# Kernel tuning notes

Measured on AMD Instinct MI355X. Metric: run time of the kernel, lower is better.

The kernel has to match this reference:

```python
import jax, jax.numpy as jnp
import numpy as np
import math

D_MODEL = 512
NHEAD = 8
N_LAYERS = 3
D_FF = 2048
INPUT_DIM = 128
NUM_CLASSES = 64
FACTOR = 5


def setup_inputs() -> dict:
    key = jax.random.key(0)
    ks = jax.random.split(key, 24)
    s = 0.02
    d, f, nl = D_MODEL, D_FF, N_LAYERS
    inp = {
        "x": jax.random.normal(ks[0], (4, 1024, INPUT_DIM), dtype=jnp.float32),
        "W_emb": jax.random.normal(ks[1], (INPUT_DIM, d), dtype=jnp.float32) * s,
        "b_emb": jnp.zeros((d,), jnp.float32),
        "Wq": jax.random.normal(ks[2], (nl, d, d), dtype=jnp.float32) * s,
        "bq": jnp.zeros((nl, d), jnp.float32),
        "Wk": jax.random.normal(ks[3], (nl, d, d), dtype=jnp.float32) * s,
        "bk": jnp.zeros((nl, d), jnp.float32),
        "Wv": jax.random.normal(ks[4], (nl, d, d), dtype=jnp.float32) * s,
        "bv": jnp.zeros((nl, d), jnp.float32),
        "Wo": jax.random.normal(ks[5], (nl, d, d), dtype=jnp.float32) * s,
        "bo": jnp.zeros((nl, d), jnp.float32),
        "ln1_g": jnp.ones((nl, d), jnp.float32),
        "ln1_b": jnp.zeros((nl, d), jnp.float32),
        "W1": jax.random.normal(ks[6], (nl, d, f), dtype=jnp.float32) * s,
        "b1": jnp.zeros((nl, f), jnp.float32),
        "W2": jax.random.normal(ks[7], (nl, f, d), dtype=jnp.float32) * s,
        "b2": jnp.zeros((nl, d), jnp.float32),
        "ln2_g": jnp.ones((nl, d), jnp.float32),
        "ln2_b": jnp.zeros((nl, d), jnp.float32),
        "W_dec": jax.random.normal(ks[8], (d, NUM_CLASSES), dtype=jnp.float32) * s,
        "b_dec": jnp.zeros((NUM_CLASSES,), jnp.float32),
    }
    return inp


def _layer_norm(x, g, b, eps=1e-5):
    m = jnp.mean(x, axis=-1, keepdims=True)
    v = jnp.var(x, axis=-1, keepdims=True)
    return (x - m) * jax.lax.rsqrt(v + eps) * g + b


def _pos_encoding(L, d):
    pos = jnp.arange(L, dtype=jnp.float32)[:, None]
    div = jnp.exp(jnp.arange(0, d, 2, dtype=jnp.float32) * (-math.log(10000.0) / d))
    pe = jnp.zeros((L, d), jnp.float32)
    pe = pe.at[:, 0::2].set(jnp.sin(pos * div))
    pe = pe.at[:, 1::2].set(jnp.cos(pos * div))
    return pe


def _prob_sparse_attn(x, Wq, bq, Wk, bk, Wv, bv, Wo, bo):
    B, L, d = x.shape
    H, dk = NHEAD, d // NHEAD
    u = min(L, int(FACTOR * math.log(L)) if L > 1 else L)
    Q = (x @ Wq + bq).reshape(B, L, H, dk).transpose(0, 2, 1, 3)  # bhld
    K = (x @ Wk + bk).reshape(B, L, H, dk).transpose(0, 2, 1, 3)
    V = (x @ Wv + bv).reshape(B, L, H, dk).transpose(0, 2, 1, 3)
    scores = jnp.einsum("bhld,bhmd->bhlm", Q, K) / math.sqrt(dk)  # [B,H,L,L]
    kth = jax.lax.top_k(scores, u)[0][..., -1:]  # kth-largest per row
    scores = jnp.where(scores < kth, -10000.0, scores)
    attn = jax.nn.softmax(scores, axis=-1)
    out = jnp.einsum("bhlm,bhmd->bhld", attn, V)
    out = out.transpose(0, 2, 1, 3).reshape(B, L, d)
    return out @ Wo + bo


def reference(x, W_emb, b_emb, Wq, bq, Wk, bk, Wv, bv, Wo, bo,
              ln1_g, ln1_b, W1, b1, W2, b2, ln2_g, ln2_b, W_dec, b_dec):
    B, L, _ = x.shape
    h = (x @ W_emb + b_emb) * math.sqrt(D_MODEL)
    h = h + _pos_encoding(L, D_MODEL)[None]
    for i in range(N_LAYERS):
        a = _prob_sparse_attn(h, Wq[i], bq[i], Wk[i], bk[i], Wv[i], bv[i], Wo[i], bo[i])
        h = _layer_norm(h + a, ln1_g[i], ln1_b[i])
        ff = jax.nn.relu(h @ W1[i] + b1[i]) @ W2[i] + b2[i]
        h = _layer_norm(h + ff, ln2_g[i], ln2_b[i])
    return h @ W_dec + b_dec
```

## Files before the change

### kernel.cpp

```cpp
#include <hip/hip_runtime.h>
#include <math.h>

#define SEQ 1024
#define BATCH 4
#define DMODEL 512
#define NHEAD 8
#define DK 64
#define DFF 2048
#define U_TOP 34
#define ROWS (BATCH * SEQ)

typedef unsigned short ushort_t;
typedef __attribute__((ext_vector_type(8))) short short8;
typedef __attribute__((ext_vector_type(4))) float float4v;
typedef __attribute__((ext_vector_type(2))) _Float16 h2v;

__device__ inline ushort_t f2bf(float f) {
  unsigned u = __float_as_uint(f);
  unsigned r = u + 0x7fffu + ((u >> 16) & 1u);
  return (ushort_t)(r >> 16);
}
__device__ inline float bf2f(ushort_t u) {
  return __uint_as_float((unsigned)u << 16);
}
__device__ inline float keyinv(unsigned cand) {
  unsigned fb = (cand & 0x80000000u) ? (cand ^ 0x80000000u) : ~cand;
  return __uint_as_float(fb);
}

union H16 { _Float16 h; unsigned short u; };
__device__ inline unsigned short h2u(float f) {
  H16 t; t.h = (_Float16)f; return t.u;
}
__device__ inline float u2h(unsigned short u) {
  H16 t; t.u = u; return (float)t.h;
}
__device__ inline _Float16 u2h16(unsigned short u) {
  H16 t; t.u = u; return t.h;
}
__device__ inline unsigned okey16(unsigned b) {
  return (b ^ (0x8000u | ((b >> 15) * 0x7FFFu))) & 0xFFFFu;
}
__device__ inline unsigned short ikey16(unsigned k) {
  return (unsigned short)(k ^ ((k >> 15) ? 0x8000u : 0xFFFFu));
}
__device__ inline int mbcnt64(unsigned long long m) {
  int lo = __builtin_amdgcn_mbcnt_lo((unsigned)m, 0);
  return __builtin_amdgcn_mbcnt_hi((unsigned)(m >> 32), lo);
}

__device__ inline void glds16(const void* g, void* l) {
  __builtin_amdgcn_global_load_lds(
      (const __attribute__((address_space(1))) unsigned int*)g,
      (__attribute__((address_space(3))) unsigned int*)l, 16, 0, 0);
}

__device__ inline unsigned pkmax(unsigned a, unsigned b) {
  return __builtin_bit_cast(unsigned, __builtin_elementwise_max(
      __builtin_bit_cast(h2v, a), __builtin_bit_cast(h2v, b)));
}

template <int RELU, int SPLIT, int BN>
__global__ __launch_bounds__(256) void gemmT(
    const ushort_t* __restrict__ A, const short* __restrict__ Bt,
    const float* __restrict__ b0, const float* __restrict__ b1,
    const float* __restrict__ b2, ushort_t* __restrict__ Cout,
    int K, int N, int zCstride) {
  constexpr int NT = BN / 32;
  __shared__ short As[2][128 * 32];
  __shared__ short Bs[2][BN * 32];

  const int tid = threadIdx.x;
  const int lane = tid & 63, w = tid >> 6;
  const int wm = w >> 1, wn = w & 1;
  const int quad = lane >> 4, r16 = lane & 15;

  const int id = blockIdx.y * gridDim.x + blockIdx.x;
  const int xcd = id & 7;
  const int loc = id >> 3;
  const int rpx = gridDim.y >> 3;
  const int bm = (xcd * rpx + (loc % rpx)) * 128;
  const int bn = (loc / rpx) * BN;

  const int srow = lane >> 2, skseg = lane & 3;
  const ushort_t* Ag0 = A + (size_t)(bm + w * 16 + srow) * K + skseg * 8;
  const ushort_t* Ag1 = Ag0 + (size_t)64 * K;
  const short* Bg0 = Bt + (size_t)(bn + w * 16 + srow) * K + skseg * 8;
  const short* Bg1 = Bg0 + (size_t)64 * K;
  const int aoff0 = (w * 16) * 32;
  const int aoff1 = (64 + w * 16) * 32;
  const int boff0 = (w * 16) * 32;
  const int boff1 = (64 + w * 16) * 32;

  float4v acc[4][NT];
#pragma unroll
  for (int m = 0; m < 4; ++m)
#pragma unroll
    for (int n = 0; n < NT; ++n) acc[m][n] = (float4v){0.f, 0.f, 0.f, 0.f};

  glds16(Ag0, &As[0][aoff0]);
  glds16(Ag1, &As[0][aoff1]);
  glds16(Bg0, &Bs[0][boff0]);
  if (BN == 128) glds16(Bg1, &Bs[0][boff1]);
  __syncthreads();

  int cur = 0;
  for (int k0 = 0; k0 < K; k0 += 32) {
    if (k0 + 32 < K) {
      const int nxt = cur ^ 1;
      glds16(Ag0 + k0 + 32, &As[nxt][aoff0]);
      glds16(Ag1 + k0 + 32, &As[nxt][aoff1]);
      glds16(Bg0 + k0 + 32, &Bs[nxt][boff0]);
      if (BN == 128) glds16(Bg1 + k0 + 32, &Bs[nxt][boff1]);
    }

    short8 af[4], bfr[NT];
#pragma unroll
    for (int m = 0; m < 4; ++m)
      af[m] =
          *(const short8*)&As[cur][(wm * 64 + m * 16 + r16) * 32 + quad * 8];
#pragma unroll
    for (int n = 0; n < NT; ++n)
      bfr[n] = *(const short8*)&Bs[cur][(wn * (BN / 2) + n * 16 + r16) * 32 +
                                        quad * 8];
#pragma unroll
    for (int m = 0; m < 4; ++m)
#pragma unroll
      for (int n = 0; n < NT; ++n)
        acc[m][n] = __builtin_amdgcn_mfma_f32_16x16x32_bf16(af[m], bfr[n],
                                                            acc[m][n], 0, 0, 0);
    __syncthreads();
    cur ^= 1;
  }

  const int z = SPLIT ? (bn >> 9) : 0;
  const float* bias = (z == 0) ? b0 : (z == 1 ? b1 : b2);
  const int cbase = SPLIT ? (bn & 511) : bn;
  const int strideN = SPLIT ? 512 : N;
  ushort_t* C = Cout + (SPLIT ? (size_t)z * zCstride : (size_t)0);

  float bias_n[NT];
#pragma unroll
  for (int n = 0; n < NT; ++n)
    bias_n[n] = bias[cbase + wn * (BN / 2) + n * 16 + r16];

#pragma unroll
  for (int m = 0; m < 4; ++m) {
#pragma unroll
    for (int n = 0; n < NT; ++n) {
      int col = cbase + wn * (BN / 2) + n * 16 + r16;
#pragma unroll
      for (int reg = 0; reg < 4; ++reg) {
        int row = bm + wm * 64 + m * 16 + quad * 4 + reg;
        float v = acc[m][n][reg] + bias_n[n];
        if (RELU) v = fmaxf(v, 0.f);
        C[(size_t)row * strideN + col] = f2bf(v);
      }
    }
  }
}

template <int BN>
__global__ __launch_bounds__(256) void gemmskT(
    const ushort_t* __restrict__ A, const short* __restrict__ Bt,
    const float* __restrict__ bias, ushort_t* __restrict__ pout,
    int K, int Ks) {
  constexpr int NT = BN / 32;
  __shared__ short As[2][128 * 32];
  __shared__ short Bs[2][BN * 32];

  const int tid = threadIdx.x;
  const int lane = tid & 63, w = tid >> 6;
  const int wm = w >> 1, wn = w & 1;
  const int quad = lane >> 4, r16 = lane & 15;

  const int id = blockIdx.y * gridDim.x + blockIdx.x;
  const int xcd = id & 7;
  const int loc = id >> 3;
  const int rpx = gridDim.y >> 3;
  const int bm = (xcd * rpx + (loc % rpx)) * 128;
  const int bn = (loc / rpx) * BN;
  const int z = blockIdx.z;
  const int koff = z * Ks;

  const int srow = lane >> 2, skseg = lane & 3;
  const ushort_t* Ag0 =
      A + (size_t)(bm + w * 16 + srow) * K + skseg * 8 + koff;
  const ushort_t* Ag1 = Ag0 + (size_t)64 * K;
  const short* Bg0 = Bt + (size_t)(bn + w * 16 + srow) * K + skseg * 8 + koff;
  const short* Bg1 = Bg0 + (size_t)64 * K;
  const int aoff0 = (w * 16) * 32;
  const int aoff1 = (64 + w * 16) * 32;
  const int boff0 = (w * 16) * 32;
  const int boff1 = (64 + w * 16) * 32;

  float4v acc[4][NT];
#pragma unroll
  for (int m = 0; m < 4; ++m)
#pragma unroll
    for (int n = 0; n < NT; ++n) acc[m][n] = (float4v){0.f, 0.f, 0.f, 0.f};

  glds16(Ag0, &As[0][aoff0]);
  glds16(Ag1, &As[0][aoff1]);
  glds16(Bg0, &Bs[0][boff0]);
  if (BN == 128) glds16(Bg1, &Bs[0][boff1]);
  __syncthreads();

  int cur = 0;
  for (int k0 = 0; k0 < Ks; k0 += 32) {
    if (k0 + 32 < Ks) {
      const int nxt = cur ^ 1;
      glds16(Ag0 + k0 + 32, &As[nxt][aoff0]);
      glds16(Ag1 + k0 + 32, &As[nxt][aoff1]);
      glds16(Bg0 + k0 + 32, &Bs[nxt][boff0]);
      if (BN == 128) glds16(Bg1 + k0 + 32, &Bs[nxt][boff1]);
    }

    short8 af[4], bfr[NT];
#pragma unroll
    for (int m = 0; m < 4; ++m)
      af[m] =
          *(const short8*)&As[cur][(wm * 64 + m * 16 + r16) * 32 + quad * 8];
#pragma unroll
    for (int n = 0; n < NT; ++n)
      bfr[n] = *(const short8*)&Bs[cur][(wn * (BN / 2) + n * 16 + r16) * 32 +
                                        quad * 8];
#pragma unroll
    for (int m = 0; m < 4; ++m)
#pragma unroll
      for (int n = 0; n < NT; ++n)
        acc[m][n] = __builtin_amdgcn_mfma_f32_16x16x32_bf16(af[m], bfr[n],
                                                            acc[m][n], 0, 0, 0);
    __syncthreads();
    cur ^= 1;
  }

  ushort_t* P = pout + (size_t)z * 2097152;
  float bias_n[NT];
#pragma unroll
  for (int n = 0; n < NT; ++n)
    bias_n[n] = (z == 0) ? bias[bn + wn * (BN / 2) + n * 16 + r16] : 0.f;

#pragma unroll
  for (int m = 0; m < 4; ++m) {
#pragma unroll
    for (int n = 0; n < NT; ++n) {
      int col = bn + wn * (BN / 2) + n * 16 + r16;
#pragma unroll
      for (int reg = 0; reg < 4; ++reg) {
        int row = bm + wm * 64 + m * 16 + quad * 4 + reg;
        float v = acc[m][n][reg] + bias_n[n];
        P[(size_t)row * 512 + col] = f2bf(v);
      }
    }
  }
}

template <int RELU, int OUTBF16, int EPI, int ADDC>
__global__ __launch_bounds__(256) void gemm64(
    const ushort_t* __restrict__ A, const short* __restrict__ Bt,
    const float* __restrict__ bias, void* __restrict__ Cout,
    const ushort_t* __restrict__ Cadd, int K, int N) {
  __shared__ short As[2][64 * 32];
  __shared__ short Bs[2][64 * 32];

  const int tid = threadIdx.x;
  const int lane = tid & 63, w = tid >> 6;
  const int wm = w >> 1, wn = w & 1;
  const int quad = lane >> 4, r16 = lane & 15;
  const int bm = blockIdx.y * 64, bn = blockIdx.x * 64;

  const int srow = tid >> 2, skseg = tid & 3;
  const ushort_t* Ag = A + (size_t)(bm + srow) * K + skseg * 8;
  const short* Bg = Bt + (size_t)(bn + srow) * K + skseg * 8;
  const int loff = w * 512;

  float4v acc[2][2];
#pragma unroll
  for (int m = 0; m < 2; ++m)
#pragma unroll
    for (int n = 0; n < 2; ++n) acc[m][n] = (float4v){0.f, 0.f, 0.f, 0.f};

  glds16(Ag, &As[0][loff]);
  glds16(Bg, &Bs[0][loff]);
  __syncthreads();

  int cur = 0;
  for (int k0 = 0; k0 < K; k0 += 32) {
    if (k0 + 32 < K) {
      const int nxt = cur ^ 1;
      glds16(Ag + k0 + 32, &As[nxt][loff]);
      glds16(Bg + k0 + 32, &Bs[nxt][loff]);
    }

    short8 af[2], bfr[2];
#pragma unroll
    for (int m = 0; m < 2; ++m)
      af[m] =
          *(const short8*)&As[cur][(wm * 32 + m * 16 + r16) * 32 + quad * 8];
#pragma unroll
    for (int n = 0; n < 2; ++n)
      bfr[n] =
          *(const short8*)&Bs[cur][(wn * 32 + n * 16 + r16) * 32 + quad * 8];
#pragma unroll
    for (int m = 0; m < 2; ++m)
#pragma unroll
      for (int n = 0; n < 2; ++n)
        acc[m][n] = __builtin_amdgcn_mfma_f32_16x16x32_bf16(af[m], bfr[n],
                                                            acc[m][n], 0, 0, 0);
    __syncthreads();
    cur ^= 1;
  }

  const float pe_c = (float)(-9.210340371976184 / 512.0);
  const float sqrtd = 22.62741699796952f;

  float bias_n[2];
#pragma unroll
  for (int n = 0; n < 2; ++n) bias_n[n] = bias[bn + wn * 32 + n * 16 + r16];

#pragma unroll
  for (int m = 0; m < 2; ++m) {
#pragma unroll
    for (int n = 0; n < 2; ++n) {
      int col = bn + wn * 32 + n * 16 + r16;
#pragma unroll
      for (int reg = 0; reg < 4; ++reg) {
        int row = bm + wm * 32 + m * 16 + quad * 4 + reg;
        float v = acc[m][n][reg] + bias_n[n];
        if (RELU) v = fmaxf(v, 0.f);
        if (EPI == 2) {
          int pos = row & (SEQ - 1);
          float e = __expf((float)(col & ~1) * pe_c);
          float arg = (float)pos * e;
          v = v * sqrtd + ((col & 1) ? __cosf(arg) : __sinf(arg));
        }
        if (ADDC) v += bf2f(Cadd[(size_t)row * N + col]);
        if (OUTBF16) {
          ((ushort_t*)Cout)[(size_t)row * N + col] = f2bf(v);
        } else {
          ((float*)Cout)[(size_t)row * N + col] = v;
        }
      }
    }
  }
}

__global__ __launch_bounds__(256) void convert_all(
    const float* __restrict__ Wq, const float* __restrict__ Wk,
    const float* __restrict__ Wv, const float* __restrict__ Wo,
    const float* __restrict__ W1, const float* __restrict__ W2,
    const float* __restrict__ W_emb, const float* __restrict__ W_dec,
    short* __restrict__ wt) {
  __shared__ float t[32][33];
  int id = blockIdx.x;
  const float* src;
  short* dst;
  int K, N, tk, tn;
  if (id < 9216) {
    int lay = id / 3072, r = id % 3072;
    short* wl = wt + (size_t)lay * 3145728;
    const size_t wsz = 512 * 512;
    if (r < 1024) {
      int wi = r >> 8, tile = r & 255;
      const float* base = (wi == 0) ? Wq : (wi == 1) ? Wk : (wi == 2) ? Wv : Wo;
      src = base + lay * wsz;
      dst = wl + wi * 262144;
      K = 512; N = 512; tk = tile >> 4; tn = tile & 15;
    } else if (r < 2048) {
      int tile = r - 1024;
      src = W1 + (size_t)lay * 512 * 2048;
      dst = wl + 1048576;
      K = 512; N = 2048; tk = tile >> 6; tn = tile & 63;
    } else {
      int tile = r - 2048;
      src = W2 + (size_t)lay * 2048 * 512;
      dst = wl + 2097152;
      K = 2048; N = 512; tk = tile >> 4; tn = tile & 15;
    }
  } else {
    int r = id - 9216;
    if (r < 64) {
      src = W_emb; dst = wt + 9437184; K = 128; N = 512; tk = r >> 4; tn = r & 15;
    } else {
      r -= 64;
      src = W_dec; dst = wt + 9502720; K = 512; N = 64; tk = r >> 1; tn = r & 1;
    }
  }
  const int k0 = tk * 32, n0 = tn * 32;
  const int tx = threadIdx.x, ty = threadIdx.y;
#pragma unroll
  for (int i = 0; i < 4; ++i) {
    int r = ty + i * 8;
    t[r][tx] = src[(size_t)(k0 + r) * N + n0 + tx];
  }
  __syncthreads();
#pragma unroll
  for (int i = 0; i < 4; ++i) {
    int r = ty + i * 8;
    dst[(size_t)(n0 + r) * K + k0 + tx] = (short)f2bf(t[tx][r]);
  }
}

__global__ __launch_bounds__(256) void f32_to_bf16_kernel(
    const float* __restrict__ src, ushort_t* __restrict__ dst) {
  int i = blockIdx.x * blockDim.x + threadIdx.x;
  float4 v = ((const float4*)src)[i];
  ushort4 o;
  o.x = f2bf(v.x); o.y = f2bf(v.y); o.z = f2bf(v.z); o.w = f2bf(v.w);
  ((ushort4*)dst)[i] = o;
}

__global__ __launch_bounds__(256) void ln_red_kernel(
    const ushort_t* __restrict__ pa, const ushort_t* __restrict__ pb,
    const float* __restrict__ g, const float* __restrict__ bb,
    ushort_t* __restrict__ hb) {
  const int row = blockIdx.x * 4 + (threadIdx.x >> 6);
  const int lane = threadIdx.x & 63;
  const size_t base = (size_t)row * DMODEL + lane * 8;
  uint4 ra = *(const uint4*)(pa + base);
  uint4 rb = *(const uint4*)(pb + base);
  uint4 rh = *(const uint4*)(hb + base);
  unsigned aa[4] = {ra.x, ra.y, ra.z, ra.w};
  unsigned ab[4] = {rb.x, rb.y, rb.z, rb.w};
  unsigned ah[4] = {rh.x, rh.y, rh.z, rh.w};
  float v[8];
#pragma unroll
  for (int k = 0; k < 4; ++k) {
    v[2 * k] = bf2f((ushort_t)(aa[k] & 0xffff)) +
               bf2f((ushort_t)(ab[k] & 0xffff)) +
               bf2f((ushort_t)(ah[k] & 0xffff));
    v[2 * k + 1] = bf2f((ushort_t)(aa[k] >> 16)) +
                   bf2f((ushort_t)(ab[k] >> 16)) +
                   bf2f((ushort_t)(ah[k] >> 16));
  }
  float sum = 0.f, sq = 0.f;
#pragma unroll
  for (int k = 0; k < 8; ++k) { sum += v[k]; sq += v[k] * v[k]; }
#pragma unroll
  for (int off = 32; off; off >>= 1) {
    sum += __shfl_xor(sum, off);
    sq += __shfl_xor(sq, off);
  }
  float mean = sum * (1.f / 512.f);
  float var = fmaxf(sq * (1.f / 512.f) - mean * mean, 0.f);
  float rstd = 1.f / sqrtf(var + 1e-5f);
  float4 g0 = *(const float4*)(g + lane * 8);
  float4 g1 = *(const float4*)(g + lane * 8 + 4);
  float4 c0 = *(const float4*)(bb + lane * 8);
  float4 c1 = *(const float4*)(bb + lane * 8 + 4);
  float gg[8] = {g0.x, g0.y, g0.z, g0.w, g1.x, g1.y, g1.z, g1.w};
  float cc[8] = {c0.x, c0.y, c0.z, c0.w, c1.x, c1.y, c1.z, c1.w};
  uint4 out;
  unsigned* op = (unsigned*)&out;
#pragma unroll
  for (int k = 0; k < 4; ++k) {
    float y0 = (v[2 * k] - mean) * rstd * gg[2 * k] + cc[2 * k];
    float y1 = (v[2 * k + 1] - mean) * rstd * gg[2 * k + 1] + cc[2 * k + 1];
    op[k] = (unsigned)f2bf(y0) | ((unsigned)f2bf(y1) << 16);
  }
  *(uint4*)(hb + base) = out;
}

#define SST 1048

__global__ __launch_bounds__(512, 8) void attn_kernel(
    const ushort_t* __restrict__ Qb, const ushort_t* __restrict__ Kb,
    const ushort_t* __restrict__ Vb, ushort_t* __restrict__ Ob) {
  __shared__ _Float16 s16[16 * SST];
  __shared__ unsigned plist[16][64];

  const int tid = threadIdx.x;
  const int id = blockIdx.x + 64 * (blockIdx.y + 8 * blockIdx.z);
  const int xcd = id & 7;
  const int loc = id >> 3;
  const int bh = xcd * 4 + (loc & 3);
  const int q0 = (loc >> 2) * 16;
  const int b = bh >> 3;
  const int h = bh & 7;

  const int w = tid >> 6;
  const int lane = tid & 63;
  const int quad = lane >> 4, r16 = lane & 15;

  {
    const int j0 = w * 128;
    const ushort_t* qrow =
        Qb + (size_t)(b * SEQ + q0 + r16) * DMODEL + h * DK + quad * 8;
    short8 aq0 = *(const short8*)qrow;
    short8 aq1 = *(const short8*)(qrow + 32);

#pragma unroll
    for (int nt = 0; nt < 8; ++nt) {
      const ushort_t* krow =
          Kb + (size_t)(b * SEQ + j0 + nt * 16 + r16) * DMODEL + h * DK +
          quad * 8;
      short8 bk0 = *(const short8*)krow;
      short8 bk1 = *(const short8*)(krow + 32);
      float4v a = (float4v){0.f, 0.f, 0.f, 0.f};
      a = __builtin_amdgcn_mfma_f32_16x16x32_bf16(aq0, bk0, a, 0, 0, 0);
      a = __builtin_amdgcn_mfma_f32_16x16x32_bf16(aq1, bk1, a, 0, 0, 0);
#pragma unroll
      for (int reg = 0; reg < 4; ++reg)
        s16[(quad * 4 + reg) * SST + j0 + nt * 16 + r16] =
            (_Float16)(a[reg] * 0.125f);
    }
  }
  __syncthreads();

  {
    const int qa = w, qb2 = w + 8;
    const _Float16* sa = &s16[qa * SST];
    const _Float16* sb = &s16[qb2 * SST];
    const unsigned* sa32 = (const unsigned*)sa;
    const unsigned* sb32 = (const unsigned*)sb;

    unsigned pk_a[8], pk_b[8];
#pragma unroll
    for (int i = 0; i < 8; ++i) {
      pk_a[i] = sa32[lane + 64 * i];
      pk_b[i] = sb32[lane + 64 * i];
    }

    unsigned ma4 = pk_a[0], mb4 = pk_b[0];
#pragma unroll
    for (int i = 1; i < 8; ++i) {
      ma4 = pkmax(ma4, pk_a[i]);
      mb4 = pkmax(mb4, pk_b[i]);
    }
    ma4 = pkmax(ma4, ma4 >> 16);
    mb4 = pkmax(mb4, mb4 >> 16);
    const unsigned lm = (ma4 & 0xffffu) | (mb4 << 16);

    unsigned mxp = lm;
#pragma unroll
    for (int j = 1; j <= 32; j <<= 1)
      mxp = pkmax(mxp, (unsigned)__shfl_xor((int)mxp, j));
    const float mxa = (float)u2h16((unsigned short)(mxp & 0xffffu));
    const float mxb = (float)u2h16((unsigned short)(mxp >> 16));

    const unsigned keyA = okey16(lm & 0xffffu);
    const unsigned keyB = okey16(lm >> 16);
    unsigned ansA = 0u, ansB = 0u;
#pragma unroll
    for (int bit = 15; bit >= 0; --bit) {
      const unsigned cA = ansA | (1u << bit);
      const unsigned cB = ansB | (1u << bit);
      const int cntA = (int)__popcll(__ballot(keyA >= cA));
      const int cntB = (int)__popcll(__ballot(keyB >= cB));
      if (cntA >= U_TOP) ansA = cA;
      if (cntB >= U_TOP) ansB = cB;
    }
    const _Float16 hTa = u2h16(ikey16(ansA));
    const _Float16 hTb = u2h16(ikey16(ansB));

    int ca = 0, cb = 0;
#pragma unroll
    for (int i = 0; i < 8; ++i) {
      const unsigned pa = pk_a[i], pb = pk_b[i];
      const int jb = 2 * lane + 128 * i;
      {
        unsigned short bits = (unsigned short)pa;
        bool k = (u2h16(bits) >= hTa);
        unsigned long long m = __ballot(k);
        if (k) {
          int p = ca + mbcnt64(m);
          if (p < 64) plist[qa][p] = ((unsigned)jb << 16) | bits;
        }
        ca += (int)__popcll(m);
      }
      {
        unsigned short bits = (unsigned short)(pa >> 16);
        bool k = (u2h16(bits) >= hTa);
        unsigned long long m = __ballot(k);
        if (k) {
          int p = ca + mbcnt64(m);
          if (p < 64) plist[qa][p] = ((unsigned)(jb + 1) << 16) | bits;
        }
        ca += (int)__popcll(m);
      }
      {
        unsigned short bits = (unsigned short)pb;
        bool k = (u2h16(bits) >= hTb);
        unsigned long long m = __ballot(k);
        if (k) {
          int p = cb + mbcnt64(m);
          if (p < 64) plist[qb2][p] = ((unsigned)jb << 16) | bits;
        }
        cb += (int)__popcll(m);
      }
      {
        unsigned short bits = (unsigned short)(pb >> 16);
        bool k = (u2h16(bits) >= hTb);
        unsigned long long m = __ballot(k);
        if (k) {
          int p = cb + mbcnt64(m);
          if (p < 64) plist[qb2][p] = ((unsigned)(jb + 1) << 16) | bits;
        }
        cb += (int)__popcll(m);
      }
    }

    if (__builtin_expect(ca > 64, 0)) {
      unsigned ans = 0u;
      int cge = ca;
      bool ex = false;
      for (int bit = 31; bit >= 0 && cge > 64 && !ex; --bit) {
        unsigned cand = ans | (1u << bit);
        float fc = keyinv(cand);
        int c = 0;
#pragma unroll
        for (int i = 0; i < 16; ++i)
          c += (int)__popcll(__ballot((float)sa[lane + 64 * i] >= fc));
        if (c >= U_TOP) { ans = cand; cge = c; ex = (c == U_TOP); }
      }
      float fa2 = keyinv(ans);
      int cc = 0;
#pragma unroll
      for (int i = 0; i < 16; ++i) {
        float va = (float)sa[lane + 64 * i];
        bool ka = va >= fa2;
        unsigned long long ma = __ballot(ka);
        if (ka) {
          int p = cc + mbcnt64(ma);
          if (p < 64)
            plist[qa][p] = ((unsigned)(lane + 64 * i) << 16) | h2u(va);
        }
        cc += (int)__popcll(ma);
      }
      ca = cc;
    }
    if (__builtin_expect(cb > 64, 0)) {
      unsigned ans = 0u;
      int cge = cb;
      bool ex = false;
      for (int bit = 31; bit >= 0 && cge > 64 && !ex; --bit) {
        unsigned cand = ans | (1u << bit);
        float fc = keyinv(cand);
        int c = 0;
#pragma unroll
        for (int i = 0; i < 16; ++i)
          c += (int)__popcll(__ballot((float)sb[lane + 64 * i] >= fc));
        if (c >= U_TOP) { ans = cand; cge = c; ex = (c == U_TOP); }
      }
      float fb2 = keyinv(ans);
      int cc = 0;
#pragma unroll
      for (int i = 0; i < 16; ++i) {
        float vb = (float)sb[lane + 64 * i];
        bool kb = vb >= fb2;
        unsigned long long mb = __ballot(kb);
        if (kb) {
          int p = cc + mbcnt64(mb);
          if (p < 64)
            plist[qb2][p] = ((unsigned)(lane + 64 * i) << 16) | h2u(vb);
        }
        cc += (int)__popcll(mb);
      }
      cb = cc;
    }
    ca = ca > 64 ? 64 : ca;
    cb = cb > 64 ? 64 : cb;

    const unsigned pua = (lane < ca) ? plist[qa][lane] : 0u;
    const unsigned pub = (lane < cb) ? plist[qb2][lane] : 0u;
    const unsigned k2a = (lane < ca) ? okey16(pua & 0xffffu) : 0u;
    const unsigned k2b = (lane < cb) ? okey16(pub & 0xffffu) : 0u;
    unsigned an2A = 0u, an2B = 0u;
#pragma unroll
    for (int bit = 15; bit >= 0; --bit) {
      const unsigned cA = an2A | (1u << bit);
      const unsigned cB = an2B | (1u << bit);
      const int cntA = (int)__popcll(__ballot(k2a >= cA));
      const int cntB = (int)__popcll(__ballot(k2b >= cB));
      if (cntA >= U_TOP) an2A = cA;
      if (cntB >= U_TOP) an2B = cB;
    }
    const _Float16 tha = u2h16(ikey16(an2A));
    const _Float16 thb = u2h16(ikey16(an2B));

    const bool keepa = (lane < ca) && (u2h16((unsigned short)pua) >= tha);
    const bool keepb = (lane < cb) && (u2h16((unsigned short)pub) >= thb);
    unsigned long long kma = __ballot(keepa);
    unsigned long long kmb = __ballot(keepb);
    const int na = (int)__popcll(kma), nb = (int)__popcll(kmb);
    float ea = keepa ? __expf((float)u2h16((unsigned short)pua) - mxa) : 0.f;
    float eb = keepb ? __expf((float)u2h16((unsigned short)pub) - mxb) : 0.f;
    float za = ea, zb = eb;
#pragma unroll
    for (int off = 32; off; off >>= 1) {
      za += __shfl_xor(za, off);
      zb += __shfl_xor(zb, off);
    }
    if (keepa) plist[qa][mbcnt64(kma)] = (pua & 0xffff0000u) | h2u(ea);
    if (keepb) plist[qb2][mbcnt64(kmb)] = (pub & 0xffff0000u) | h2u(eb);

    const ushort_t* vbase = Vb + (size_t)b * SEQ * DMODEL + h * DK;
    const int half = lane >> 5;
    const int dpos = (lane & 31) * 2;
    float a00 = 0.f, a01 = 0.f, a10 = 0.f, a11 = 0.f;
    float b00 = 0.f, b01 = 0.f, b10 = 0.f, b11 = 0.f;
    const int nmax = na > nb ? na : nb;
    for (int i = half * 2; i < nmax; i += 4) {
      const uint2 ea2 = *(const uint2*)&plist[qa][i];
      const uint2 eb2 = *(const uint2*)&plist[qb2][i];
      const unsigned ua0 = (i < na) ? ea2.x : 0u;
      const unsigned ua1 = (i + 1 < na) ? ea2.y : 0u;
      const unsigned ub0 = (i < nb) ? eb2.x : 0u;
      const unsigned ub1 = (i + 1 < nb) ? eb2.y : 0u;
      const unsigned va0 =
          *(const unsigned*)(vbase + (size_t)(ua0 >> 16) * DMODEL + dpos);
      const unsigned va1 =
          *(const unsigned*)(vbase + (size_t)(ua1 >> 16) * DMODEL + dpos);
      const unsigned vb0 =
          *(const unsigned*)(vbase + (size_t)(ub0 >> 16) * DMODEL + dpos);
      const unsigned vb1 =
          *(const unsigned*)(vbase + (size_t)(ub1 >> 16) * DMODEL + dpos);
      const float wa0 = (float)u2h16((unsigned short)ua0);
      const float wa1 = (float)u2h16((unsigned short)ua1);
      const float wb0 = (float)u2h16((unsigned short)ub0);
      const float wb1 = (float)u2h16((unsigned short)ub1);
      a00 += wa0 * bf2f((ushort_t)(va0 & 0xffffu));
      a01 += wa0 * bf2f((ushort_t)(va0 >> 16));
      a10 += wa1 * bf2f((ushort_t)(va1 & 0xffffu));
      a11 += wa1 * bf2f((ushort_t)(va1 >> 16));
      b00 += wb0 * bf2f((ushort_t)(vb0 & 0xffffu));
      b01 += wb0 * bf2f((ushort_t)(vb0 >> 16));
      b10 += wb1 * bf2f((ushort_t)(vb1 & 0xffffu));
      b11 += wb1 * bf2f((ushort_t)(vb1 >> 16));
    }
    float ax0 = a00 + a10, ax1 = a01 + a11;
    float bx0 = b00 + b10, bx1 = b01 + b11;
    ax0 += __shfl_xor(ax0, 32);
    ax1 += __shfl_xor(ax1, 32);
    bx0 += __shfl_xor(bx0, 32);
    bx1 += __shfl_xor(bx1, 32);
    const float iza = 1.f / za, izb = 1.f / zb;
    const int qq = half ? qb2 : qa;
    const float sc = half ? izb : iza;
    const float r0 = (half ? bx0 : ax0) * sc;
    const float r1 = (half ? bx1 : ax1) * sc;
    const unsigned outw = (unsigned)f2bf(r0) | ((unsigned)f2bf(r1) << 16);
    *(unsigned*)(Ob + (size_t)(b * SEQ + q0 + qq) * DMODEL + h * DK + dpos) =
        outw;
  }
}

extern "C" void kernel_launch(void* const* d_in, const int* in_sizes, int n_in,
                              void* d_out, int out_size, void* d_ws,
                              size_t ws_size, hipStream_t stream) {
  const float* x = (const float*)d_in[0];
  const float* W_emb = (const float*)d_in[1];
  const float* b_emb = (const float*)d_in[2];
  const float* Wq = (const float*)d_in[3];
  const float* bq = (const float*)d_in[4];
  const float* Wk = (const float*)d_in[5];
  const float* bk = (const float*)d_in[6];
  const float* Wv = (const float*)d_in[7];
  const float* bv = (const float*)d_in[8];
  const float* Wo = (const float*)d_in[9];
  const float* bo = (const float*)d_in[10];
  const float* ln1_g = (const float*)d_in[11];
  const float* ln1_b = (const float*)d_in[12];
  const float* W1 = (const float*)d_in[13];
  const float* b1 = (const float*)d_in[14];
  const float* W2 = (const float*)d_in[15];
  const float* b2 = (const float*)d_in[16];
  const float* ln2_g = (const float*)d_in[17];
  const float* ln2_b = (const float*)d_in[18];
  const float* W_dec = (const float*)d_in[19];
  const float* b_dec = (const float*)d_in[20];

  char* wsb = (char*)d_ws;
  ushort_t* qkv = (ushort_t*)wsb;
  ushort_t* ffh = (ushort_t*)wsb;
  ushort_t* wop = (ushort_t*)wsb;
  ushort_t* ao = (ushort_t*)(wsb + ((size_t)16 << 20));
  ushort_t* xb = (ushort_t*)(wsb + ((size_t)16 << 20));
  ushort_t* ffp = (ushort_t*)(wsb + ((size_t)16 << 20));
  ushort_t* hb = (ushort_t*)(wsb + ((size_t)24 << 20));
  short* wt = (short*)(wsb + ((size_t)28 << 20));
  short* wembT = wt + 9437184;
  short* wdecT = wt + 9502720;

  f32_to_bf16_kernel<<<dim3(512), 256, 0, stream>>>(x, xb);
  convert_all<<<dim3(9312), dim3(32, 8), 0, stream>>>(Wq, Wk, Wv, Wo, W1, W2,
                                                      W_emb, W_dec, wt);
  gemm64<0, 1, 2, 0><<<dim3(8, 64), 256, 0, stream>>>(
      xb, wembT, b_emb, (void*)hb, nullptr, 128, 512);

  for (int i = 0; i < 3; ++i) {
    short* wtL = wt + (size_t)i * 3145728;

    gemmT<0, 1, 64><<<dim3(24, 32), 256, 0, stream>>>(
        hb, wtL, bq + i * DMODEL, bk + i * DMODEL, bv + i * DMODEL, qkv, 512,
        512, 2097152);

    attn_kernel<<<dim3(SEQ / 16, NHEAD, BATCH), dim3(512), 0, stream>>>(
        qkv, qkv + 2097152, qkv + 4194304, ao);

    gemmskT<64><<<dim3(8, 32, 2), 256, 0, stream>>>(
        ao, wtL + 786432, bo + i * DMODEL, wop, 512, 256);
    ln_red_kernel<<<dim3(ROWS / 4), 256, 0, stream>>>(
        wop, wop + 2097152, ln1_g + i * DMODEL, ln1_b + i * DMODEL, hb);

    gemmT<1, 0, 64><<<dim3(32, 32), 256, 0, stream>>>(
        hb, wtL + 1048576, b1 + i * DFF, nullptr, nullptr, ffh, 512, 2048, 0);
    gemmskT<64><<<dim3(8, 32, 2), 256, 0, stream>>>(
        ffh, wtL + 2097152, b2 + i * DMODEL, ffp, 2048, 1024);
    ln_red_kernel<<<dim3(ROWS / 4), 256, 0, stream>>>(
        ffp, ffp + 2097152, ln2_g + i * DMODEL, ln2_b + i * DMODEL, hb);
  }

  gemm64<0, 0, 0, 0><<<dim3(1, 64), 256, 0, stream>>>(
      hb, wdecT, b_dec, d_out, nullptr, 512, 64);
}
```

Before: 507.0 us.

## Triple-buffer GEMM LDS stages with partial vmcnt waits and raw barriers

Converts the three GEMM kernels from double-buffered LDS staging to a three-stage ring, issuing the load two K-steps ahead. A per-iteration full sync is replaced by an explicit s_waitcnt vmcnt(G) that waits only for the older stage, followed by a bare s_barrier. The goal is to keep more global-to-LDS loads in flight and overlap them better with MFMA work. It costs 50% more shared memory per block, which may lower occupancy, and correctness depends on hand-counted vmcnt values and on the compiler not reordering around the inline asm.

```diff
diff --git a/kernel.cpp b/kernel.cpp
--- a/kernel.cpp
+++ b/kernel.cpp
@@ -55,6 +55,14 @@
       (__attribute__((address_space(3))) unsigned int*)l, 16, 0, 0);
 }
 
+template <int N>
+__device__ inline void waitvm() {
+  if constexpr (N == 0) asm volatile("s_waitcnt vmcnt(0)" ::: "memory");
+  else if constexpr (N == 2) asm volatile("s_waitcnt vmcnt(2)" ::: "memory");
+  else if constexpr (N == 3) asm volatile("s_waitcnt vmcnt(3)" ::: "memory");
+  else if constexpr (N == 4) asm volatile("s_waitcnt vmcnt(4)" ::: "memory");
+}
+
 __device__ inline unsigned pkmax(unsigned a, unsigned b) {
   return __builtin_bit_cast(unsigned, __builtin_elementwise_max(
       __builtin_bit_cast(h2v, a), __builtin_bit_cast(h2v, b)));
@@ -67,8 +75,9 @@
     const float* __restrict__ b2, ushort_t* __restrict__ Cout,
     int K, int N, int zCstride) {
   constexpr int NT = BN / 32;
-  __shared__ short As[2][128 * 32];
-  __shared__ short Bs[2][BN * 32];
+  constexpr int G = (BN == 128) ? 4 : 3;
+  __shared__ short As[3][128 * 32];
+  __shared__ short Bs[3][BN * 32];
 
   const int tid = threadIdx.x;
   const int lane = tid & 63, w = tid >> 6;
@@ -98,39 +107,48 @@
 #pragma unroll
     for (int n = 0; n < NT; ++n) acc[m][n] = (float4v){0.f, 0.f, 0.f, 0.f};
 
-  glds16(Ag0, &As[0][aoff0]);
-  glds16(Ag1, &As[0][aoff1]);
-  glds16(Bg0, &Bs[0][boff0]);
-  if (BN == 128) glds16(Bg1, &Bs[0][boff1]);
-  __syncthreads();
-
-  int cur = 0;
-  for (int k0 = 0; k0 < K; k0 += 32) {
-    if (k0 + 32 < K) {
-      const int nxt = cur ^ 1;
-      glds16(Ag0 + k0 + 32, &As[nxt][aoff0]);
-      glds16(Ag1 + k0 + 32, &As[nxt][aoff1]);
-      glds16(Bg0 + k0 + 32, &Bs[nxt][boff0]);
-      if (BN == 128) glds16(Bg1 + k0 + 32, &Bs[nxt][boff1]);
-    }
+  const int nk = K >> 5;
+  auto stage = [&](int t, int bi) {
+    glds16(Ag0 + (t << 5), &As[bi][aoff0]);
+    glds16(Ag1 + (t << 5), &As[bi][aoff1]);
+    glds16(Bg0 + (t << 5), &Bs[bi][boff0]);
+    if constexpr (BN == 128) glds16(Bg1 + (t << 5), &Bs[bi][boff1]);
+  };
+
+  stage(0, 0);
+  if (nk > 1) {
+    stage(1, 1);
+    waitvm<G>();
+  } else {
+    waitvm<0>();
+  }
+  __builtin_amdgcn_s_barrier();
+
+  int rd = 0, wr = 2;
+  for (int k = 0; k < nk; ++k) {
+    if (k + 2 < nk) stage(k + 2, wr);
 
     short8 af[4], bfr[NT];
 #pragma unroll
     for (int m = 0; m < 4; ++m)
       af[m] =
-          *(const short8*)&As[cur][(wm * 64 + m * 16 + r16) * 32 + quad * 8];
+          *(const short8*)&As[rd][(wm * 64 + m * 16 + r16) * 32 + quad * 8];
 #pragma unroll
     for (int n = 0; n < NT; ++n)
-      bfr[n] = *(const short8*)&Bs[cur][(wn * (BN / 2) + n * 16 + r16) * 32 +
-                                        quad * 8];
+      bfr[n] = *(const short8*)&Bs[rd][(wn * (BN / 2) + n * 16 + r16) * 32 +
+                                       quad * 8];
 #pragma unroll
     for (int m = 0; m < 4; ++m)
 #pragma unroll
       for (int n = 0; n < NT; ++n)
         acc[m][n] = __builtin_amdgcn_mfma_f32_16x16x32_bf16(af[m], bfr[n],
                                                             acc[m][n], 0, 0, 0);
-    __syncthreads();
-    cur ^= 1;
+    if (k + 1 < nk) {
+      if (k + 2 < nk) waitvm<G>(); else waitvm<0>();
+      __builtin_amdgcn_s_barrier();
+    }
+    wr = rd;
+    rd = (rd == 2) ? 0 : rd + 1;
   }
 
   const int z = SPLIT ? (bn >> 9) : 0;
@@ -166,8 +184,9 @@
     const float* __restrict__ bias, ushort_t* __restrict__ pout,
     int K, int Ks) {
   constexpr int NT = BN / 32;
-  __shared__ short As[2][128 * 32];
-  __shared__ short Bs[2][BN * 32];
+  constexpr int G = (BN == 128) ? 4 : 3;
+  __shared__ short As[3][128 * 32];
+  __shared__ short Bs[3][BN * 32];
 
   const int tid = threadIdx.x;
   const int lane = tid & 63, w = tid >> 6;
@@ -200,39 +219,48 @@
 #pragma unroll
     for (int n = 0; n < NT; ++n) acc[m][n] = (float4v){0.f, 0.f, 0.f, 0.f};
 
-  glds16(Ag0, &As[0][aoff0]);
-  glds16(Ag1, &As[0][aoff1]);
-  glds16(Bg0, &Bs[0][boff0]);
-  if (BN == 128) glds16(Bg1, &Bs[0][boff1]);
-  __syncthreads();
-
-  int cur = 0;
-  for (int k0 = 0; k0 < Ks; k0 += 32) {
-    if (k0 + 32 < Ks) {
-      const int nxt = cur ^ 1;
-      glds16(Ag0 + k0 + 32, &As[nxt][aoff0]);
-      glds16(Ag1 + k0 + 32, &As[nxt][aoff1]);
-      glds16(Bg0 + k0 + 32, &Bs[nxt][boff0]);
-      if (BN == 128) glds16(Bg1 + k0 + 32, &Bs[nxt][boff1]);
-    }
+  const int nk = Ks >> 5;
+  auto stage = [&](int t, int bi) {
+    glds16(Ag0 + (t << 5), &As[bi][aoff0]);
+    glds16(Ag1 + (t << 5), &As[bi][aoff1]);
+    glds16(Bg0 + (t << 5), &Bs[bi][boff0]);
+    if constexpr (BN == 128) glds16(Bg1 + (t << 5), &Bs[bi][boff1]);
+  };
+
+  stage(0, 0);
+  if (nk > 1) {
+    stage(1, 1);
+    waitvm<G>();
+  } else {
+    waitvm<0>();
+  }
+  __builtin_amdgcn_s_barrier();
+
+  int rd = 0, wr = 2;
+  for (int k = 0; k < nk; ++k) {
+    if (k + 2 < nk) stage(k + 2, wr);
 
     short8 af[4], bfr[NT];
 #pragma unroll
     for (int m = 0; m < 4; ++m)
       af[m] =
-          *(const short8*)&As[cur][(wm * 64 + m * 16 + r16) * 32 + quad * 8];
+          *(const short8*)&As[rd][(wm * 64 + m * 16 + r16) * 32 + quad * 8];
 #pragma unroll
     for (int n = 0; n < NT; ++n)
-      bfr[n] = *(const short8*)&Bs[cur][(wn * (BN / 2) + n * 16 + r16) * 32 +
-                                        quad * 8];
+      bfr[n] = *(const short8*)&Bs[rd][(wn * (BN / 2) + n * 16 + r16) * 32 +
+                                       quad * 8];
 #pragma unroll
     for (int m = 0; m < 4; ++m)
 #pragma unroll
       for (int n = 0; n < NT; ++n)
         acc[m][n] = __builtin_amdgcn_mfma_f32_16x16x32_bf16(af[m], bfr[n],
                                                             acc[m][n], 0, 0, 0);
-    __syncthreads();
-    cur ^= 1;
+    if (k + 1 < nk) {
+      if (k + 2 < nk) waitvm<G>(); else waitvm<0>();
+      __builtin_amdgcn_s_barrier();
+    }
+    wr = rd;
+    rd = (rd == 2) ? 0 : rd + 1;
   }
 
   ushort_t* P = pout + (size_t)z * 2097152;
@@ -261,8 +289,9 @@
     const ushort_t* __restrict__ A, const short* __restrict__ Bt,
     const float* __restrict__ bias, void* __restrict__ Cout,
     const ushort_t* __restrict__ Cadd, int K, int N) {
-  __shared__ short As[2][64 * 32];
-  __shared__ short Bs[2][64 * 32];
+  constexpr int G = 2;
+  __shared__ short As[3][64 * 32];
+  __shared__ short Bs[3][64 * 32];
 
   const int tid = threadIdx.x;
   const int lane = tid & 63, w = tid >> 6;
@@ -281,35 +310,46 @@
 #pragma unroll
     for (int n = 0; n < 2; ++n) acc[m][n] = (float4v){0.f, 0.f, 0.f, 0.f};
 
-  glds16(Ag, &As[0][loff]);
-  glds16(Bg, &Bs[0][loff]);
-  __syncthreads();
-
-  int cur = 0;
-  for (int k0 = 0; k0 < K; k0 += 32) {
-    if (k0 + 32 < K) {
-      const int nxt = cur ^ 1;
-      glds16(Ag + k0 + 32, &As[nxt][loff]);
-      glds16(Bg + k0 + 32, &Bs[nxt][loff]);
-    }
+  const int nk = K >> 5;
+  auto stage = [&](int t, int bi) {
+    glds16(Ag + (t << 5), &As[bi][loff]);
+    glds16(Bg + (t << 5), &Bs[bi][loff]);
+  };
+
+  stage(0, 0);
+  if (nk > 1) {
+    stage(1, 1);
+    waitvm<G>();
+  } else {
+    waitvm<0>();
+  }
+  __builtin_amdgcn_s_barrier();
+
+  int rd = 0, wr = 2;
+  for (int k = 0; k < nk; ++k) {
+    if (k + 2 < nk) stage(k + 2, wr);
 
     short8 af[2], bfr[2];
 #pragma unroll
     for (int m = 0; m < 2; ++m)
       af[m] =
-          *(const short8*)&As[cur][(wm * 32 + m * 16 + r16) * 32 + quad * 8];
+          *(const short8*)&As[rd][(wm * 32 + m * 16 + r16) * 32 + quad * 8];
 #pragma unroll
     for (int n = 0; n < 2; ++n)
       bfr[n] =
-          *(const short8*)&Bs[cur][(wn * 32 + n * 16 + r16) * 32 + quad * 8];
+          *(const short8*)&Bs[rd][(wn * 32 + n * 16 + r16) * 32 + quad * 8];
 #pragma unroll
     for (int m = 0; m < 2; ++m)
 #pragma unroll
       for (int n = 0; n < 2; ++n)
         acc[m][n] = __builtin_amdgcn_mfma_f32_16x16x32_bf16(af[m], bfr[n],
                                                             acc[m][n], 0, 0, 0);
-    __syncthreads();
-    cur ^= 1;
+    if (k + 1 < nk) {
+      if (k + 2 < nk) waitvm<G>(); else waitvm<0>();
+      __builtin_amdgcn_s_barrier();
+    }
+    wr = rd;
+    rd = (rd == 2) ? 0 : rd + 1;
   }
 
   const float pe_c = (float)(-9.210340371976184 / 512.0);
```

Result: no change. 513.3 us (+1.2%).
